# Optimization experiments

Measured on AMD Instinct MI355X. Metric: run time of the kernel, lower is better.

## Reference

```python
import jax, jax.numpy as jnp
import numpy as np

# ---- layer_param constants (ihmehimmeli alpha-synapse defaults, see shape_source) ----
K_NO_SPIKE = 1000.0
DECAY_RATE = 1.0          # K in exp(K*t)
DECAY_RATE_INV = 1.0
FIRE_THRESHOLD = 1.0
IN_FEATURES = 1024
OUT_FEATURES = 512
N_PULSE = 10
BATCH = 32
MIN_W_ARG = -0.3678794411714423  # -1/e, domain boundary of Lambert W0


def lambertw0(x):
    """Principal branch Lambert W on [-1/e, 0], via Halley iterations."""
    e = jnp.exp(1.0)
    # series init near the branch point, w ~= x for small |x|
    w = jnp.where(x < -0.25,
                  -1.0 + jnp.sqrt(jnp.maximum(2.0 * (1.0 + e * x), 0.0)),
                  x * (1.0 - x))
    def halley(w, _):
        ew = jnp.exp(w)
        f = w * ew - x
        denom = ew * (w + 1.0) - (w + 2.0) * f / (2.0 * (w + 1.0) + 1e-12)
        w = w - f / (denom + 1e-12)
        return w, None
    w, _ = jax.lax.scan(halley, w, None, length=12)
    return w


def _alpha_solve(act, weight):
    """Causal-set cumulative spike-time solve for alpha synapses.
    act: [B,N] input spike times, weight: [O,N].
    V(t) = e^{-K t} (A t - B) with A = sum w e^{K t_i}, B = sum w t_i e^{K t_i};
    threshold crossing: t* = B/A - W0(-theta*K/A * e^{K B/A})/K,
    valid if t* lies between the last included and the next input spike.
    """
    order = jnp.argsort(act, axis=1)                             # [B,N]
    t_s = jnp.take_along_axis(act, order, axis=1)                # sorted spike times
    valid_in = t_s < K_NO_SPIKE
    z = jnp.where(valid_in, jnp.exp(DECAY_RATE * t_s), 0.0)      # exp of valid sorted spikes
    w_s = weight[:, order].transpose(1, 0, 2)                    # [B,O,N] weights in sorted order
    A_c = jnp.cumsum(w_s * z[:, None, :], axis=2)                # causal-set cumulative A
    B_c = jnp.cumsum(w_s * (z * t_s)[:, None, :], axis=2)        # causal-set cumulative B
    A_pos = A_c > 1e-10
    A_safe = jnp.where(A_pos, A_c, 1.0)
    b_over_a = B_c / A_safe
    arg = -FIRE_THRESHOLD * DECAY_RATE / A_safe * jnp.exp(jnp.minimum(DECAY_RATE * b_over_a, 80.0))
    lam_ok = A_pos & (arg >= MIN_W_ARG)
    wl = lambertw0(jnp.clip(arg, MIN_W_ARG, 0.0))
    t_cand = b_over_a - wl * DECAY_RATE_INV
    next_t = jnp.concatenate([t_s[:, 1:], jnp.full_like(t_s[:, :1], K_NO_SPIKE)], axis=1)
    valid = (lam_ok & valid_in[:, None, :]
             & (t_cand >= t_s[:, None, :]) & (t_cand <= next_t[:, None, :]))
    k_star = jnp.argmax(valid, axis=2)                           # first causal set that fires
    spiked = jnp.any(valid, axis=2)
    take = lambda m: jnp.take_along_axis(m, k_star[:, :, None], axis=2)[:, :, 0]
    spike_time = jnp.where(spiked, take(t_cand), K_NO_SPIKE)
    A = jnp.where(spiked, take(A_c), 1.0)
    Bv = jnp.where(spiked, take(B_c), 0.0)
    Wv = jnp.where(spiked, take(wl), 0.0)
    rank = jnp.argsort(order, axis=1)                            # position of each input in sorted order
    causal = rank[:, None, :] <= k_star[:, :, None]              # [B,O,N]
    return spike_time, A, Bv, Wv, causal


def setup_inputs() -> dict:
    key = jax.random.key(0)
    k1, k2 = jax.random.split(key)
    x = jax.random.uniform(k1, (BATCH, IN_FEATURES), dtype=jnp.float32)
    std = float(np.sqrt(2.0 / (IN_FEATURES + OUT_FEATURES)))
    weight = std * 7.0 + std * jax.random.normal(k2, (OUT_FEATURES, IN_FEATURES + N_PULSE), dtype=jnp.float32)
    pulse = jnp.linspace(0.0, 1.0, N_PULSE + 2, dtype=jnp.float32)[1:-1]
    return {"x": x, "weight": weight, "pulse": pulse}


def reference(x, weight, pulse):
    act = jnp.concatenate([x, jnp.broadcast_to(pulse[None, :], (x.shape[0], N_PULSE))], axis=1)
    spike_time, _, _, _, _ = _alpha_solve(act, weight)
    return spike_time
```

## Files before the change

### kernel.cpp

```cpp
#include <hip/hip_runtime.h>
#include <math.h>

#define IN_FEATURES 1024
#define OUT_FEATURES 512
#define N_PULSE 10
#define NCOL 1034
#define BATCH 32
#define MIN_W_ARG -0.3678794411714423
#define CH 16
#define NK 1040
#define NPAD 1056

#define OFF_TS  (NPAD * 4)
#define OFF_Z   (NPAD * 8)
#define OFF_ZT  (NPAD * 16)
#define TBL_BYTES (NPAD * 24)

__global__ __launch_bounds__(256, 1) void transpose_w(const float* __restrict__ w,
                                                      float* __restrict__ wT) {
    __shared__ float tile[64][65];
    const int n0 = (blockIdx.x % 17) * 64;
    const int o0 = (blockIdx.x / 17) * 64;
    const int tx = threadIdx.x & 63, ty = threadIdx.x >> 6;
    #pragma unroll
    for (int r = 0; r < 16; ++r) {
        int ol = r * 4 + ty;
        int n = n0 + tx;
        if (n < NCOL) tile[ol][tx] = w[(o0 + ol) * NCOL + n];
    }
    __syncthreads();
    #pragma unroll
    for (int r = 0; r < 16; ++r) {
        int nl = r * 4 + ty;
        int n = n0 + nl;
        if (n < NCOL) wT[n * OUT_FEATURES + o0 + tx] = tile[tx][nl];
    }
}

__global__ __launch_bounds__(128, 1) void rank_sort(
        const float* __restrict__ x, const float* __restrict__ pulse,
        char* __restrict__ tbl) {
    __shared__ unsigned long long sk[NPAD];
    __shared__ float keyf[NCOL];
    const int b = blockIdx.x / 9, part = blockIdx.x % 9;
    const int tid = threadIdx.x;

    for (int e = tid; e < NPAD; e += 128) {
        if (e < NCOL) {
            float t = (e < IN_FEATURES) ? x[b * IN_FEATURES + e]
                                        : pulse[e - IN_FEATURES];
            unsigned u = __float_as_uint(t);
            u = (u & 0x80000000u) ? ~u : (u | 0x80000000u);
            sk[e] = ((unsigned long long)u << 11) | (unsigned)e;
            keyf[e] = t;
        } else {
            sk[e] = 0xFFFFFFFFFFFFFFFFULL;
        }
    }
    __syncthreads();

    char* base = tbl + b * TBL_BYTES;
    int*    ordg = (int*)base;
    float*  tsg  = (float*)(base + OFF_TS);
    double* zg   = (double*)(base + OFF_Z);
    double* ztg  = (double*)(base + OFF_ZT);

    const int e = part * 128 + tid;
    if (e < NCOL) {
        unsigned long long mk = sk[e];
        int r = 0;
        for (int j0 = 0; j0 < NPAD; j0 += 16) {
            unsigned long long c[16];
            #pragma unroll
            for (int i = 0; i < 16; ++i) c[i] = sk[j0 + i];
            #pragma unroll
            for (int i = 0; i < 16; ++i) r += (c[i] < mk);
        }
        float t = keyf[e];
        double zv = exp((double)t);
        ordg[r] = e; tsg[r] = t; zg[r] = zv; ztg[r] = zv * (double)t;
    }
    if (part == 8 && tid >= 10) {
        int p = NCOL + (tid - 10);
        if (p < NPAD) { ordg[p] = 0; tsg[p] = -1.0f; zg[p] = 0.0; ztg[p] = 0.0; }
    }
}

__device__ __forceinline__ double lambertw0(double xx) {
    const double e = 2.718281828459045;
    double w = (xx < -0.25) ? (-1.0 + sqrt(fmax(2.0 * (1.0 + e * xx), 0.0)))
                            : xx * (1.0 - xx);
    #pragma unroll 4
    for (int i = 0; i < 12; ++i) {
        double ew = exp(w);
        double f  = w * ew - xx;
        double denom = ew * (w + 1.0) - (w + 2.0) * f / (2.0 * (w + 1.0) + 1e-12);
        w = w - f / (denom + 1e-12);
    }
    return w;
}

__global__ __launch_bounds__(64, 1) void solve_kernel(
        const float* __restrict__ wT,
        const char* __restrict__ tbl,
        float* __restrict__ out) {
    __shared__ char smem[TBL_BYTES];
    const int b = blockIdx.x >> 3;
    const int o = ((blockIdx.x & 7) << 6) | threadIdx.x;

    {
        const uint4* g = (const uint4*)(tbl + b * TBL_BYTES);
        uint4* l = (uint4*)smem;
        #pragma unroll 4
        for (int e = threadIdx.x; e < TBL_BYTES / 16; e += 64) l[e] = g[e];
    }
    __syncthreads();
    const int*    ord_l = (const int*)smem;
    const float*  ts_l  = (const float*)(smem + OFF_TS);
    const double* z_l   = (const double*)(smem + OFF_Z);
    const double* zt_l  = (const double*)(smem + OFF_ZT);

    double A = 0.0, Bv = 0.0, fA = 0.0, fB = 0.0;
    int fk = 0;
    bool done = false;
    float bufA[CH], bufB[CH];

    auto gather = [&](float* buf, int k0) {
        int idx[CH];
        #pragma unroll
        for (int i = 0; i < CH; ++i) idx[i] = ord_l[k0 + i];
        #pragma unroll
        for (int i = 0; i < CH; ++i) buf[i] = wT[idx[i] * OUT_FEATURES + o];
    };
    auto step = [&](const float* buf, int k0) {
        double tz[CH + 1], tzt[CH];
        float  tts[CH + 1];
        #pragma unroll
        for (int i = 0; i <= CH; ++i) tz[i] = z_l[k0 + i];
        #pragma unroll
        for (int i = 0; i < CH; ++i) tzt[i] = zt_l[k0 + i];
        #pragma unroll
        for (int i = 0; i <= CH; ++i) tts[i] = ts_l[k0 + i];
        #pragma unroll
        for (int i = 0; i < CH; ++i) {
            double w = (double)buf[i];
            A  = fma(w, tz[i],  A);
            Bv = fma(w, tzt[i], Bv);
            bool fire = (!done) & (A > 1e-10) &
                        (fma(A, (double)tts[i + 1], -Bv) >= tz[i + 1]);
            if (fire) { fA = A; fB = Bv; fk = k0 + i; done = true; }
        }
    };

    gather(bufA, 0);
    for (int k0 = 0; k0 < NK; k0 += 2 * CH) {
        gather(bufB, k0 + CH);
        step(bufA, k0);
        if (__ballot(!done) == 0ULL) break;
        if (k0 + 2 * CH < NK) gather(bufA, k0 + 2 * CH);
        step(bufB, k0 + CH);
        if (__ballot(!done) == 0ULL) break;
    }

    double AA, BB, tk, tn;
    bool have;
    if (done) {
        AA = fA; BB = fB;
        tk = (double)ts_l[fk];
        tn = (fk == NCOL - 1) ? 1000.0 : (double)ts_l[fk + 1];
        have = true;
    } else {
        AA = A; BB = Bv;
        tk = (double)ts_l[NCOL - 1];
        tn = 1000.0;
        have = (AA > 1e-10);
    }
    float result = 1000.0f;
    bool need_fb = false;
    if (have) {
        double boa = BB / AA;
        double arg = -exp(fmin(boa, 80.0)) / AA;
        if (arg >= MIN_W_ARG) {
            double wl = lambertw0(fmin(fmax(arg, MIN_W_ARG), 0.0));
            double tc = boa - wl;
            if (tc >= tk && tc <= tn) result = (float)tc;
            else need_fb = done;
        } else need_fb = done;
    }

    if (__ballot(need_fb) != 0ULL) {
        double A2 = fA, B2 = fB;
        for (int k = fk + 1; k < NCOL; ++k) {
            if (!need_fb) break;
            double w = (double)wT[ord_l[k] * OUT_FEATURES + o];
            A2 = fma(w, z_l[k], A2);
            B2 = fma(w, zt_l[k], B2);
            if (!(A2 > 1e-10)) continue;
            double tkk = (double)ts_l[k];
            double tnn = (k == NCOL - 1) ? 1000.0 : (double)ts_l[k + 1];
            double boa = B2 / A2;
            double arg = -exp(fmin(boa, 80.0)) / A2;
            if (arg >= MIN_W_ARG) {
                double wl = lambertw0(fmin(fmax(arg, MIN_W_ARG), 0.0));
                double tc = boa - wl;
                if (tc >= tkk && tc <= tnn) { result = (float)tc; need_fb = false; }
            }
        }
    }
    out[b * OUT_FEATURES + o] = result;
}

extern "C" void kernel_launch(void* const* d_in, const int* in_sizes, int n_in,
                              void* d_out, int out_size, void* d_ws, size_t ws_size,
                              hipStream_t stream) {
    const float* x      = (const float*)d_in[0];
    const float* weight = (const float*)d_in[1];
    const float* pulse  = (const float*)d_in[2];
    float* out = (float*)d_out;

    char* ws = (char*)d_ws;
    float* wT = (float*)ws;
    char*  tbl = ws + (size_t)NCOL * OUT_FEATURES * 4;

    hipLaunchKernelGGL(transpose_w, dim3(17 * 8), dim3(256), 0, stream, weight, wT);
    hipLaunchKernelGGL(rank_sort,   dim3(BATCH * 9), dim3(128), 0, stream, x, pulse, tbl);
    hipLaunchKernelGGL(solve_kernel, dim3(BATCH * OUT_FEATURES / 64), dim3(64), 0, stream,
                       wT, tbl, out);
}
```

Baseline: 90.17 us.

## Split causal-set scan across 16 waves with segmented prefix and merge transpose/rank kernels

The solve kernel now uses 1024 threads per block: each of 16 waves owns a 66-element segment of the sorted inputs, computes segment sums of A and B, then rescans its segment with the prefix offsets to find its first firing index. Wave 0 then picks the minimum firing index and runs the Lambert-W solve and fallback. Previously a single wave scanned serially with early exit. Separately, the transpose and rank kernels are fused into one launch to save a kernel launch. The trade-off is that early exit is lost, since every segment is read twice, in exchange for much more parallelism across the 256 blocks.

```diff
diff --git a/kernel.cpp b/kernel.cpp
--- a/kernel.cpp
+++ b/kernel.cpp
@@ -1,5 +1,6 @@
 #include <hip/hip_runtime.h>
 #include <math.h>
+#include <limits.h>
 
 #define IN_FEATURES 1024
 #define OUT_FEATURES 512
@@ -7,82 +8,91 @@
 #define NCOL 1034
 #define BATCH 32
 #define MIN_W_ARG -0.3678794411714423
-#define CH 16
-#define NK 1040
-#define NPAD 1056
-
-#define OFF_TS  (NPAD * 4)
-#define OFF_Z   (NPAD * 8)
-#define OFF_ZT  (NPAD * 16)
-#define TBL_BYTES (NPAD * 24)
-
-__global__ __launch_bounds__(256, 1) void transpose_w(const float* __restrict__ w,
-                                                      float* __restrict__ wT) {
-    __shared__ float tile[64][65];
-    const int n0 = (blockIdx.x % 17) * 64;
-    const int o0 = (blockIdx.x / 17) * 64;
-    const int tx = threadIdx.x & 63, ty = threadIdx.x >> 6;
-    #pragma unroll
-    for (int r = 0; r < 16; ++r) {
-        int ol = r * 4 + ty;
-        int n = n0 + tx;
-        if (n < NCOL) tile[ol][tx] = w[(o0 + ol) * NCOL + n];
-    }
-    __syncthreads();
-    #pragma unroll
-    for (int r = 0; r < 16; ++r) {
-        int nl = r * 4 + ty;
-        int n = n0 + nl;
-        if (n < NCOL) wT[n * OUT_FEATURES + o0 + tx] = tile[tx][nl];
-    }
-}
-
-__global__ __launch_bounds__(128, 1) void rank_sort(
+
+#define NSEG 16
+#define SEG 66
+#define SCAN (NSEG * SEG)
+#define TBLN 1088
+
+#define OFF_TS  (TBLN * 4)
+#define OFF_Z   (TBLN * 8)
+#define OFF_ZT  (TBLN * 16)
+#define TBL_BYTES (TBLN * 24)
+
+#define PREP_T_BLOCKS 136
+#define PREP_R_PARTS 5
+#define PREP_BLOCKS (PREP_T_BLOCKS + BATCH * PREP_R_PARTS)
+
+__global__ __launch_bounds__(256, 1) void prep_kernel(
+        const float* __restrict__ w, float* __restrict__ wT,
         const float* __restrict__ x, const float* __restrict__ pulse,
         char* __restrict__ tbl) {
-    __shared__ unsigned long long sk[NPAD];
-    __shared__ float keyf[NCOL];
-    const int b = blockIdx.x / 9, part = blockIdx.x % 9;
+    __shared__ char smem_u[64 * 65 * 4];
     const int tid = threadIdx.x;
 
-    for (int e = tid; e < NPAD; e += 128) {
+    if (blockIdx.x < PREP_T_BLOCKS) {
+        float (*tile)[65] = (float (*)[65])smem_u;
+        const int n0 = (blockIdx.x % 17) * 64;
+        const int o0 = (blockIdx.x / 17) * 64;
+        const int tx = tid & 63, ty = tid >> 6;
+        #pragma unroll
+        for (int r = 0; r < 16; ++r) {
+            int ol = r * 4 + ty, n = n0 + tx;
+            if (n < NCOL) tile[ol][tx] = w[(o0 + ol) * NCOL + n];
+        }
+        __syncthreads();
+        #pragma unroll
+        for (int r = 0; r < 16; ++r) {
+            int nl = r * 4 + ty, n = n0 + nl;
+            if (n < NCOL) wT[n * OUT_FEATURES + o0 + tx] = tile[tx][nl];
+        }
+    } else {
+        unsigned long long* sk = (unsigned long long*)smem_u;
+        float* keyf = (float*)(smem_u + TBLN * 8);
+        const int rb = blockIdx.x - PREP_T_BLOCKS;
+        const int b = rb / PREP_R_PARTS, part = rb % PREP_R_PARTS;
+
+        for (int e = tid; e < TBLN; e += 256) {
+            if (e < NCOL) {
+                float t = (e < IN_FEATURES) ? x[b * IN_FEATURES + e]
+                                            : pulse[e - IN_FEATURES];
+                unsigned u = __float_as_uint(t);
+                u = (u & 0x80000000u) ? ~u : (u | 0x80000000u);
+                sk[e] = ((unsigned long long)u << 11) | (unsigned)e;
+                keyf[e] = t;
+            } else {
+                sk[e] = 0xFFFFFFFFFFFFFFFFULL;
+            }
+        }
+        __syncthreads();
+
+        char* base = tbl + b * TBL_BYTES;
+        int*    ordg = (int*)base;
+        float*  tsg  = (float*)(base + OFF_TS);
+        double* zg   = (double*)(base + OFF_Z);
+        double* ztg  = (double*)(base + OFF_ZT);
+
+        const int e = part * 256 + tid;
         if (e < NCOL) {
-            float t = (e < IN_FEATURES) ? x[b * IN_FEATURES + e]
-                                        : pulse[e - IN_FEATURES];
-            unsigned u = __float_as_uint(t);
-            u = (u & 0x80000000u) ? ~u : (u | 0x80000000u);
-            sk[e] = ((unsigned long long)u << 11) | (unsigned)e;
-            keyf[e] = t;
-        } else {
-            sk[e] = 0xFFFFFFFFFFFFFFFFULL;
-        }
-    }
-    __syncthreads();
-
-    char* base = tbl + b * TBL_BYTES;
-    int*    ordg = (int*)base;
-    float*  tsg  = (float*)(base + OFF_TS);
-    double* zg   = (double*)(base + OFF_Z);
-    double* ztg  = (double*)(base + OFF_ZT);
-
-    const int e = part * 128 + tid;
-    if (e < NCOL) {
-        unsigned long long mk = sk[e];
-        int r = 0;
-        for (int j0 = 0; j0 < NPAD; j0 += 16) {
-            unsigned long long c[16];
-            #pragma unroll
-            for (int i = 0; i < 16; ++i) c[i] = sk[j0 + i];
-            #pragma unroll
-            for (int i = 0; i < 16; ++i) r += (c[i] < mk);
-        }
-        float t = keyf[e];
-        double zv = exp((double)t);
-        ordg[r] = e; tsg[r] = t; zg[r] = zv; ztg[r] = zv * (double)t;
-    }
-    if (part == 8 && tid >= 10) {
-        int p = NCOL + (tid - 10);
-        if (p < NPAD) { ordg[p] = 0; tsg[p] = -1.0f; zg[p] = 0.0; ztg[p] = 0.0; }
+            unsigned long long mk = sk[e];
+            int r = 0;
+            for (int j0 = 0; j0 < TBLN; j0 += 16) {
+                unsigned long long c[16];
+                #pragma unroll
+                for (int i = 0; i < 16; ++i) c[i] = sk[j0 + i];
+                #pragma unroll
+                for (int i = 0; i < 16; ++i) r += (c[i] < mk);
+            }
+            float t = keyf[e];
+            double zv = exp((double)t);
+            ordg[r] = e; tsg[r] = t; zg[r] = zv; ztg[r] = zv * (double)t;
+        }
+        if (part == PREP_R_PARTS - 1) {
+            int p = 1024 + tid;
+            if (p >= NCOL && p < TBLN) {
+                ordg[p] = 0; tsg[p] = -1.0f; zg[p] = 0.0; ztg[p] = 0.0;
+            }
+        }
     }
 }
 
@@ -100,19 +110,25 @@
     return w;
 }
 
-__global__ __launch_bounds__(64, 1) void solve_kernel(
+__global__ __launch_bounds__(1024) void solve_kernel(
         const float* __restrict__ wT,
         const char* __restrict__ tbl,
         float* __restrict__ out) {
     __shared__ char smem[TBL_BYTES];
+    __shared__ double segA[NSEG * 64], segB[NSEG * 64];
+    __shared__ int    sfk[NSEG * 64];
+    __shared__ double sfA[NSEG * 64], sfB[NSEG * 64];
+
     const int b = blockIdx.x >> 3;
-    const int o = ((blockIdx.x & 7) << 6) | threadIdx.x;
+    const int o0 = (blockIdx.x & 7) << 6;
+    const int wave = threadIdx.x >> 6;
+    const int lane = threadIdx.x & 63;
+    const int o = o0 + lane;
 
     {
         const uint4* g = (const uint4*)(tbl + b * TBL_BYTES);
         uint4* l = (uint4*)smem;
-        #pragma unroll 4
-        for (int e = threadIdx.x; e < TBL_BYTES / 16; e += 64) l[e] = g[e];
+        for (int e = threadIdx.x; e < TBL_BYTES / 16; e += 1024) l[e] = g[e];
     }
     __syncthreads();
     const int*    ord_l = (const int*)smem;
@@ -120,94 +136,120 @@
     const double* z_l   = (const double*)(smem + OFF_Z);
     const double* zt_l  = (const double*)(smem + OFF_ZT);
 
-    double A = 0.0, Bv = 0.0, fA = 0.0, fB = 0.0;
-    int fk = 0;
-    bool done = false;
-    float bufA[CH], bufB[CH];
-
-    auto gather = [&](float* buf, int k0) {
-        int idx[CH];
+    const int k0 = wave * SEG;
+
+    {
+        double a0 = 0.0, a1 = 0.0, b0 = 0.0, b1 = 0.0;
+        for (int c = 0; c < SEG; c += 11) {
+            int idx[11]; float buf[11];
+            #pragma unroll
+            for (int i = 0; i < 11; ++i) idx[i] = ord_l[k0 + c + i];
+            #pragma unroll
+            for (int i = 0; i < 11; ++i) buf[i] = wT[idx[i] * OUT_FEATURES + o];
+            #pragma unroll
+            for (int i = 0; i < 11; ++i) {
+                double w = (double)buf[i];
+                if (i & 1) { a1 = fma(w, z_l[k0 + c + i], a1);
+                             b1 = fma(w, zt_l[k0 + c + i], b1); }
+                else       { a0 = fma(w, z_l[k0 + c + i], a0);
+                             b0 = fma(w, zt_l[k0 + c + i], b0); }
+            }
+        }
+        segA[wave * 64 + lane] = a0 + a1;
+        segB[wave * 64 + lane] = b0 + b1;
+    }
+    __syncthreads();
+
+    {
+        double A = 0.0, Bv = 0.0;
+        for (int s = 0; s < wave; ++s) {
+            A  += segA[s * 64 + lane];
+            Bv += segB[s * 64 + lane];
+        }
+        int fk = INT_MAX; double fA = 0.0, fB = 0.0;
+        for (int c = 0; c < SEG; c += 11) {
+            int idx[11]; float buf[11];
+            #pragma unroll
+            for (int i = 0; i < 11; ++i) idx[i] = ord_l[k0 + c + i];
+            #pragma unroll
+            for (int i = 0; i < 11; ++i) buf[i] = wT[idx[i] * OUT_FEATURES + o];
+            #pragma unroll
+            for (int i = 0; i < 11; ++i) {
+                int k = k0 + c + i;
+                double w = (double)buf[i];
+                A  = fma(w, z_l[k],  A);
+                Bv = fma(w, zt_l[k], Bv);
+                bool fire = (fk == INT_MAX) & (A > 1e-10) &
+                            (fma(A, (double)ts_l[k + 1], -Bv) >= z_l[k + 1]);
+                if (fire) { fk = k; fA = A; fB = Bv; }
+            }
+        }
+        sfk[wave * 64 + lane] = fk;
+        sfA[wave * 64 + lane] = fA;
+        sfB[wave * 64 + lane] = fB;
+    }
+    __syncthreads();
+
+    if (wave == 0) {
+        int gk = INT_MAX; double gA = 0.0, gB = 0.0;
         #pragma unroll
-        for (int i = 0; i < CH; ++i) idx[i] = ord_l[k0 + i];
-        #pragma unroll
-        for (int i = 0; i < CH; ++i) buf[i] = wT[idx[i] * OUT_FEATURES + o];
-    };
-    auto step = [&](const float* buf, int k0) {
-        double tz[CH + 1], tzt[CH];
-        float  tts[CH + 1];
-        #pragma unroll
-        for (int i = 0; i <= CH; ++i) tz[i] = z_l[k0 + i];
-        #pragma unroll
-        for (int i = 0; i < CH; ++i) tzt[i] = zt_l[k0 + i];
-        #pragma unroll
-        for (int i = 0; i <= CH; ++i) tts[i] = ts_l[k0 + i];
-        #pragma unroll
-        for (int i = 0; i < CH; ++i) {
-            double w = (double)buf[i];
-            A  = fma(w, tz[i],  A);
-            Bv = fma(w, tzt[i], Bv);
-            bool fire = (!done) & (A > 1e-10) &
-                        (fma(A, (double)tts[i + 1], -Bv) >= tz[i + 1]);
-            if (fire) { fA = A; fB = Bv; fk = k0 + i; done = true; }
-        }
-    };
-
-    gather(bufA, 0);
-    for (int k0 = 0; k0 < NK; k0 += 2 * CH) {
-        gather(bufB, k0 + CH);
-        step(bufA, k0);
-        if (__ballot(!done) == 0ULL) break;
-        if (k0 + 2 * CH < NK) gather(bufA, k0 + 2 * CH);
-        step(bufB, k0 + CH);
-        if (__ballot(!done) == 0ULL) break;
-    }
-
-    double AA, BB, tk, tn;
-    bool have;
-    if (done) {
-        AA = fA; BB = fB;
-        tk = (double)ts_l[fk];
-        tn = (fk == NCOL - 1) ? 1000.0 : (double)ts_l[fk + 1];
-        have = true;
-    } else {
-        AA = A; BB = Bv;
-        tk = (double)ts_l[NCOL - 1];
-        tn = 1000.0;
-        have = (AA > 1e-10);
-    }
-    float result = 1000.0f;
-    bool need_fb = false;
-    if (have) {
-        double boa = BB / AA;
-        double arg = -exp(fmin(boa, 80.0)) / AA;
-        if (arg >= MIN_W_ARG) {
-            double wl = lambertw0(fmin(fmax(arg, MIN_W_ARG), 0.0));
-            double tc = boa - wl;
-            if (tc >= tk && tc <= tn) result = (float)tc;
-            else need_fb = done;
-        } else need_fb = done;
-    }
-
-    if (__ballot(need_fb) != 0ULL) {
-        double A2 = fA, B2 = fB;
-        for (int k = fk + 1; k < NCOL; ++k) {
-            if (!need_fb) break;
-            double w = (double)wT[ord_l[k] * OUT_FEATURES + o];
-            A2 = fma(w, z_l[k], A2);
-            B2 = fma(w, zt_l[k], B2);
-            if (!(A2 > 1e-10)) continue;
-            double tkk = (double)ts_l[k];
-            double tnn = (k == NCOL - 1) ? 1000.0 : (double)ts_l[k + 1];
-            double boa = B2 / A2;
-            double arg = -exp(fmin(boa, 80.0)) / A2;
+        for (int s = 0; s < NSEG; ++s) {
+            int k = sfk[s * 64 + lane];
+            if (k < gk) { gk = k; gA = sfA[s * 64 + lane]; gB = sfB[s * 64 + lane]; }
+        }
+        bool done = (gk < NCOL);
+
+        double AA, BB, tk, tn;
+        bool have;
+        if (done) {
+            AA = gA; BB = gB;
+            tk = (double)ts_l[gk];
+            tn = (double)ts_l[gk + 1];
+            have = true;
+        } else {
+            double tA = 0.0, tB = 0.0;
+            #pragma unroll
+            for (int s = 0; s < NSEG; ++s) { tA += segA[s * 64 + lane]; tB += segB[s * 64 + lane]; }
+            AA = tA; BB = tB;
+            tk = (double)ts_l[NCOL - 1];
+            tn = 1000.0;
+            have = (AA > 1e-10);
+        }
+
+        float result = 1000.0f;
+        bool need_fb = false;
+        if (have) {
+            double boa = BB / AA;
+            double arg = -exp(fmin(boa, 80.0)) / AA;
             if (arg >= MIN_W_ARG) {
                 double wl = lambertw0(fmin(fmax(arg, MIN_W_ARG), 0.0));
                 double tc = boa - wl;
-                if (tc >= tkk && tc <= tnn) { result = (float)tc; need_fb = false; }
-            }
-        }
-    }
-    out[b * OUT_FEATURES + o] = result;
+                if (tc >= tk && tc <= tn) result = (float)tc;
+                else need_fb = done;
+            } else need_fb = done;
+        }
+
+        if (__ballot(need_fb) != 0ULL) {
+            double A2 = gA, B2 = gB;
+            for (int k = gk + 1; k < NCOL && k >= 0; ++k) {
+                if (!need_fb) break;
+                double w = (double)wT[ord_l[k] * OUT_FEATURES + o];
+                A2 = fma(w, z_l[k], A2);
+                B2 = fma(w, zt_l[k], B2);
+                if (!(A2 > 1e-10)) continue;
+                double tkk = (double)ts_l[k];
+                double tnn = (k == NCOL - 1) ? 1000.0 : (double)ts_l[k + 1];
+                double boa = B2 / A2;
+                double arg = -exp(fmin(boa, 80.0)) / A2;
+                if (arg >= MIN_W_ARG) {
+                    double wl = lambertw0(fmin(fmax(arg, MIN_W_ARG), 0.0));
+                    double tc = boa - wl;
+                    if (tc >= tkk && tc <= tnn) { result = (float)tc; need_fb = false; }
+                }
+            }
+        }
+        out[b * OUT_FEATURES + o] = result;
+    }
 }
 
 extern "C" void kernel_launch(void* const* d_in, const int* in_sizes, int n_in,
@@ -222,8 +264,8 @@
     float* wT = (float*)ws;
     char*  tbl = ws + (size_t)NCOL * OUT_FEATURES * 4;
 
-    hipLaunchKernelGGL(transpose_w, dim3(17 * 8), dim3(256), 0, stream, weight, wT);
-    hipLaunchKernelGGL(rank_sort,   dim3(BATCH * 9), dim3(128), 0, stream, x, pulse, tbl);
-    hipLaunchKernelGGL(solve_kernel, dim3(BATCH * OUT_FEATURES / 64), dim3(64), 0, stream,
+    hipLaunchKernelGGL(prep_kernel, dim3(PREP_BLOCKS), dim3(256), 0, stream,
+                       weight, wT, x, pulse, tbl);
+    hipLaunchKernelGGL(solve_kernel, dim3(BATCH * OUT_FEATURES / 64), dim3(1024), 0, stream,
                        wT, tbl, out);
 }
```

Result: no change. 91.48 us (+1.5%).
